# Kernel tuning notes

Hardware: AMD Instinct MI355X
Metric: run time of the kernel (lower is better)

Reference implementation:

```python
import jax, jax.numpy as jnp
import numpy as np

B, S, T = 32, 512, 32
EMB, HID = 256, 512
VOCAB, OOV = 50000, 100


def setup_inputs() -> dict:
    key = jax.random.key(0)
    ks = jax.random.split(key, 20)
    g = lambda k, shape: (0.02 * jax.random.normal(k, shape)).astype(jnp.float32)
    return {
        "dec_input_ids": jax.random.randint(ks[0], (B, T), 0, VOCAB),
        "enc_ids_ext": jax.random.randint(ks[1], (B, S), 0, VOCAB + OOV),
        "encoder_states": jax.random.normal(ks[2], (B, S, HID), jnp.float32),
        "enc_padding_mask": jnp.ones((B, S), jnp.float32),
        "init_h": jax.random.normal(ks[3], (B, HID), jnp.float32),
        "init_c": jax.random.normal(ks[4], (B, HID), jnp.float32),
        "embeddings": g(ks[5], (VOCAB, EMB)),
        "W_enc": g(ks[6], (HID, HID)),
        "b_enc": jnp.zeros((HID,), jnp.float32),
        "W_attn": g(ks[7], (2 * HID, HID)),
        "v": g(ks[8], (HID,)),
        "w_cov": g(ks[9], (HID,)),
        "b_cov": jnp.zeros((HID,), jnp.float32),
        "W_x": g(ks[10], (EMB + HID, HID)),
        "W_out": g(ks[11], (2 * HID, HID)),
        "Wk": g(ks[12], (HID, 4 * HID)),
        "Wr": g(ks[13], (HID, 4 * HID)),
        "b_lstm": jnp.zeros((4 * HID,), jnp.float32),
        "W_pgen": g(ks[14], (4 * HID, 1)),
        "W_proj": g(ks[15], (HID, VOCAB)),
        "b_proj": jnp.zeros((VOCAB,), jnp.float32),
    }


def reference(dec_input_ids, enc_ids_ext, encoder_states, enc_padding_mask,
              init_h, init_c, embeddings, W_enc, b_enc, W_attn, v, w_cov,
              b_cov, W_x, W_out, Wk, Wr, b_lstm, W_pgen, W_proj, b_proj):
    Bq = encoder_states.shape[0]
    # 1x1 conv over [B,S,1,H] == pointwise linear
    enc_feat = jnp.einsum('bsh,hv->bsv', encoder_states, W_enc) + b_enc  # [B,S,V]
    emb = jnp.swapaxes(embeddings[dec_input_ids], 0, 1)  # [T,B,E]
    rows = jnp.arange(Bq)[:, None]

    def lstm(x, h, c):
        z = x @ Wk + h @ Wr + b_lstm
        i, f, g_, o = jnp.split(z, 4, axis=-1)
        c2 = jax.nn.sigmoid(f) * c + jax.nn.sigmoid(i) * jnp.tanh(g_)
        h2 = jax.nn.sigmoid(o) * jnp.tanh(c2)
        return h2, c2

    def attend(h, c, cov):
        dec_feat = jnp.concatenate([h, c], -1) @ W_attn  # [B,V]
        feats = enc_feat + dec_feat[:, None, :]
        if cov is not None:  # 1x1 conv on coverage [B,S,1,1] -> [B,S,V]
            feats = feats + cov[..., None] * w_cov + b_cov
        e = jnp.sum(v * jnp.tanh(feats), -1)  # [B,S]
        attn = jax.nn.softmax(e, axis=-1) * enc_padding_mask
        attn = attn / jnp.sum(attn, -1, keepdims=True)
        ctx = jnp.einsum('bs,bsv->bv', attn, enc_feat)
        return ctx, attn

    def decode(inp, h, c, ctx, cov):
        x = jnp.concatenate([inp, ctx], -1) @ W_x
        h, c = lstm(x, h, c)
        ctx, attn = attend(h, c, cov)
        p_gen = jax.nn.sigmoid(jnp.concatenate([ctx, h, c, x], -1) @ W_pgen)  # [B,1]
        out = jnp.concatenate([h, ctx], -1) @ W_out
        vocab_dist = jax.nn.softmax(out @ W_proj + b_proj, axis=-1)
        ext = jnp.concatenate([p_gen * vocab_dist,
                               jnp.zeros((Bq, OOV), vocab_dist.dtype)], -1)
        final = ext.at[rows, enc_ids_ext].add((1.0 - p_gen) * attn)
        return h, c, ctx, attn, p_gen, final

    # step 0: coverage starts as None, initialized from first attn dist
    ctx0 = jnp.zeros((Bq, HID), encoder_states.dtype)
    h, c, ctx, attn0, pg0, final0 = decode(emb[0], init_h, init_c, ctx0, None)
    cov = attn0

    def scan_step(carry, inp):
        h, c, ctx, cov = carry
        h, c, ctx, attn, pg, final = decode(inp, h, c, ctx, cov)
        return (h, c, ctx, cov + attn), final

    (_, _, _, cov), finals = jax.lax.scan(scan_step, (h, c, ctx, cov), emb[1:])
    final_dists = jnp.concatenate([final0[None], finals], axis=0)  # [T,B,VOCAB+OOV]
    return final_dists
```

## Files before the change

kernel.cpp:

```cpp
#include <hip/hip_runtime.h>
#include <math.h>

#define Bq 32
#define Sq 512
#define Tq 32
#define EMBq 256
#define HIDq 512
#define VOCABq 50000
#define OOVq 100
#define VEXTq (VOCABq + OOVq)
#define HALF_N 25088

typedef unsigned short u16;
typedef unsigned long long u64;
typedef __attribute__((ext_vector_type(8))) short bf16x8;
typedef __attribute__((ext_vector_type(4))) float f32x4;

__device__ __forceinline__ float sigmoidf_(float x){ return 1.0f/(1.0f+__expf(-x)); }
__device__ __forceinline__ float tanhf_(float x){ return 1.0f - 2.0f/(__expf(2.0f*x)+1.0f); }

__device__ __forceinline__ u16 f2bf(float x){
  union{float f; unsigned u;} v; v.f=x;
  unsigned r = v.u + 0x7FFFu + ((v.u>>16)&1u);
  return (u16)(r>>16);
}
__device__ __forceinline__ float bf2f(u16 h){
  union{unsigned u; float f;} v; v.u = ((unsigned)h)<<16; return v.f;
}

__device__ __forceinline__ float ld1(const float* p){
  return __hip_atomic_load((float*)p, __ATOMIC_RELAXED, __HIP_MEMORY_SCOPE_AGENT);
}
__device__ __forceinline__ void st1(float* p, float v){
  __hip_atomic_store(p, v, __ATOMIC_RELAXED, __HIP_MEMORY_SCOPE_AGENT);
}
__device__ __forceinline__ float2 ld2(const float* p){
  u64 v = __hip_atomic_load((u64*)p, __ATOMIC_RELAXED, __HIP_MEMORY_SCOPE_AGENT);
  union{u64 u; float2 f;} c; c.u=v; return c.f;
}
__device__ __forceinline__ void atadd(float* p, float v){
  __hip_atomic_fetch_add(p, v, __ATOMIC_RELAXED, __HIP_MEMORY_SCOPE_AGENT);
}

__device__ __forceinline__ void mbar(unsigned* gs, int sc, unsigned tag){
  asm volatile("s_waitcnt vmcnt(0)" ::: "memory");
  __syncthreads();
  if (threadIdx.x==0)
    __hip_atomic_store(gs+sc, tag, __ATOMIC_RELAXED, __HIP_MEMORY_SCOPE_AGENT);
  if (threadIdx.x<64){
    for(;;){
      unsigned v = (threadIdx.x<8)
        ? __hip_atomic_load(gs+threadIdx.x, __ATOMIC_RELAXED, __HIP_MEMORY_SCOPE_AGENT)
        : tag;
      if (__all(v>=tag)) break;
      __builtin_amdgcn_s_sleep(1);
    }
  }
  __syncthreads();
}

__device__ __forceinline__ float blockSum512(float v, float* red){
  #pragma unroll
  for (int off=32; off>0; off>>=1) v += __shfl_down(v, off);
  int lane = threadIdx.x & 63, wid = threadIdx.x >> 6;
  __syncthreads();
  if (lane==0) red[wid]=v;
  __syncthreads();
  float t=0.f;
  #pragma unroll
  for (int w=0;w<8;++w) t+=red[w];
  return t;
}

__global__ __launch_bounds__(256) void k_wet(const float* __restrict__ W, u16* __restrict__ WT){
  __shared__ float T[32][33];
  const int n0 = blockIdx.x*32, k0 = blockIdx.y*32;
  const int tid=threadIdx.x;
  #pragma unroll
  for (int it=0; it<4; ++it){
    int id = tid+it*256; int kk=id>>5, nn=id&31;
    T[kk][nn] = W[(size_t)(k0+kk)*512 + n0+nn];
  }
  __syncthreads();
  #pragma unroll
  for (int it=0; it<4; ++it){
    int id=tid+it*256; int nn=id>>5, kk=id&31;
    WT[(size_t)(n0+nn)*512 + k0+kk] = f2bf(T[kk][nn]);
  }
}

__global__ __launch_bounds__(256) void k_wkt(const float* __restrict__ Wk, u16* __restrict__ WkT){
  __shared__ float T[32][33];
  const int n0 = blockIdx.x*32, k0 = blockIdx.y*32;
  const int tid=threadIdx.x;
  #pragma unroll
  for (int it=0; it<4; ++it){
    int id=tid+it*256; int kk=id>>5, nn=id&31;
    T[kk][nn] = Wk[(size_t)(k0+kk)*2048 + n0+nn];
  }
  __syncthreads();
  #pragma unroll
  for (int it=0; it<4; ++it){
    int id=tid+it*256; int nn=id>>5, kk=id&31;
    WkT[(size_t)(n0+nn)*512 + k0+kk] = f2bf(T[kk][nn]);
  }
}

__global__ __launch_bounds__(512) void k_wx2c(const float* __restrict__ W_x,
    const float* __restrict__ Wpgen, u16* __restrict__ Xb, float* __restrict__ Wxp){
  __shared__ float red[8];
  const int j = blockIdx.x, i = threadIdx.x;
  float v = W_x[(size_t)(256+j)*512 + i];
  Xb[(size_t)j*512 + i] = f2bf(v);
  float s = blockSum512(v*Wpgen[1536+i], red);
  if (i==0) Wxp[j] = s;
}

__global__ __launch_bounds__(256) void k_gemm512(const u16* __restrict__ A,
    const u16* __restrict__ B, const float* __restrict__ bias,
    float* __restrict__ out, int ncols, int use_bias){
  __shared__ u16 As[128*40];
  __shared__ u16 Bs[128*40];
  const int tid = threadIdx.x;
  const int m0 = blockIdx.x * 128;
  const int n0 = blockIdx.y * 128;
  const int wid = tid>>6, lane = tid&63;
  const int wm = (wid>>1)*64, wn = (wid&1)*64;
  const int l15 = lane&15, l4 = lane>>4;
  f32x4 acc[4][4];
  #pragma unroll
  for (int mi=0;mi<4;++mi)
    #pragma unroll
    for (int ni=0;ni<4;++ni) acc[mi][ni] = (f32x4){0.f,0.f,0.f,0.f};
  for (int kt=0; kt<16; ++kt){
    const int k0 = kt*32;
    __syncthreads();
    #pragma unroll
    for (int it=0; it<2; ++it){
      int id = tid + it*256;
      int row = id>>2, c4 = id&3;
      uint4 va = *(const uint4*)(A + (size_t)(m0+row)*512 + k0 + c4*8);
      *(uint4*)(&As[row*40 + c4*8]) = va;
      uint4 vb = *(const uint4*)(B + (size_t)(n0+row)*512 + k0 + c4*8);
      *(uint4*)(&Bs[row*40 + c4*8]) = vb;
    }
    __syncthreads();
    bf16x8 a[4], b[4];
    #pragma unroll
    for (int mi=0;mi<4;++mi) a[mi] = *(const bf16x8*)(&As[(wm+mi*16+l15)*40 + l4*8]);
    #pragma unroll
    for (int ni=0;ni<4;++ni) b[ni] = *(const bf16x8*)(&Bs[(wn+ni*16+l15)*40 + l4*8]);
    #pragma unroll
    for (int mi=0;mi<4;++mi)
      #pragma unroll
      for (int ni=0;ni<4;++ni)
        acc[mi][ni] = __builtin_amdgcn_mfma_f32_16x16x32_bf16(a[mi], b[ni], acc[mi][ni], 0,0,0);
  }
  #pragma unroll
  for (int ni=0;ni<4;++ni){
    const int col = n0 + wn + ni*16 + l15;
    const float bp = use_bias ? bias[col] : 0.f;
    #pragma unroll
    for (int mi=0;mi<4;++mi){
      const int rbase = m0 + wm + mi*16 + l4*4;
      #pragma unroll
      for (int r=0;r<4;++r)
        out[(size_t)(rbase+r)*ncols + col] = acc[mi][ni][r] + bp;
    }
  }
}

__global__ __launch_bounds__(256) void k_encm(const float* __restrict__ es,
    const u16* __restrict__ WET, const float* __restrict__ b_enc,
    u16* __restrict__ EFbf){
  __shared__ u16 As[128*40];
  __shared__ u16 Bs[128*40];
  const int tid=threadIdx.x;
  const int m0 = blockIdx.x*128, n0 = blockIdx.y*128;
  const int wid=tid>>6, lane=tid&63;
  const int wm=(wid>>1)*64, wn=(wid&1)*64;
  const int l15=lane&15, l4=lane>>4;
  f32x4 acc[4][4];
  #pragma unroll
  for (int mi=0;mi<4;++mi)
    #pragma unroll
    for (int ni=0;ni<4;++ni) acc[mi][ni] = (f32x4){0.f,0.f,0.f,0.f};
  for (int kt=0; kt<16; ++kt){
    const int k0=kt*32;
    __syncthreads();
    #pragma unroll
    for (int it=0; it<4; ++it){
      int id=tid+it*256; int row=id>>3, q=id&7;
      float4 v = *(const float4*)(es + (size_t)(m0+row)*512 + k0 + q*4);
      u64 pk = (u64)f2bf(v.x) | ((u64)f2bf(v.y)<<16) | ((u64)f2bf(v.z)<<32) | ((u64)f2bf(v.w)<<48);
      *(u64*)&As[row*40 + q*4] = pk;
    }
    #pragma unroll
    for (int it=0; it<2; ++it){
      int id=tid+it*256; int row=id>>2, c4=id&3;
      uint4 v = *(const uint4*)(WET + (size_t)(n0+row)*512 + k0 + c4*8);
      *(uint4*)&Bs[row*40 + c4*8] = v;
    }
    __syncthreads();
    bf16x8 a[4], b[4];
    #pragma unroll
    for (int mi=0;mi<4;++mi) a[mi] = *(const bf16x8*)(&As[(wm+mi*16+l15)*40 + l4*8]);
    #pragma unroll
    for (int ni=0;ni<4;++ni) b[ni] = *(const bf16x8*)(&Bs[(wn+ni*16+l15)*40 + l4*8]);
    #pragma unroll
    for (int mi=0;mi<4;++mi)
      #pragma unroll
      for (int ni=0;ni<4;++ni)
        acc[mi][ni] = __builtin_amdgcn_mfma_f32_16x16x32_bf16(a[mi], b[ni], acc[mi][ni], 0,0,0);
  }
  #pragma unroll
  for (int ni=0;ni<4;++ni){
    const int col = n0+wn+ni*16+l15;
    const float bp = b_enc[col];
    #pragma unroll
    for (int mi=0;mi<4;++mi){
      const int rb = m0+wm+mi*16+l4*4;
      #pragma unroll
      for (int r=0;r<4;++r)
        EFbf[(size_t)(rb+r)*512 + col] = f2bf(acc[mi][ni][r]+bp);
    }
  }
}

__global__ __launch_bounds__(512) void k_embx(const int* __restrict__ dec_ids,
  const float* __restrict__ emb, const float* __restrict__ W_x,
  const float* __restrict__ Wpgen, u16* __restrict__ embx_bf, float* __restrict__ embxp){
  __shared__ float A[16][257];
  __shared__ int ids[16];
  __shared__ float red[8];
  const int tid = threadIdx.x, r0 = blockIdx.x*16;
  if (tid<16){
    int row = r0+tid, tt = row>>5, bb = row&31;
    ids[tid] = dec_ids[bb*Tq + tt];
  }
  __syncthreads();
  for (int idx=tid; idx<16*256; idx+=512){
    int rr = idx>>8, kk = idx&255;
    A[rr][kk] = emb[(size_t)ids[rr]*EMBq + kk];
  }
  __syncthreads();
  float acc[16];
  #pragma unroll
  for (int r=0;r<16;++r) acc[r]=0.f;
  for (int k=0;k<256;++k){
    float w = W_x[(size_t)k*HIDq + tid];
    #pragma unroll
    for (int r=0;r<16;++r) acc[r] += A[r][k]*w;
  }
  float wp4 = Wpgen[1536+tid];
  for (int r=0;r<16;++r){
    embx_bf[(size_t)(r0+r)*HIDq + tid] = f2bf(acc[r]);
    float s = blockSum512(acc[r]*wp4, red);
    if (tid==0) embxp[r0+r] = s;
  }
}

__global__ __launch_bounds__(512) void k_trans(const float* __restrict__ in,
    float* __restrict__ out, int K, int N){
  __shared__ float T[32][33];
  const int n0 = blockIdx.x*32, k0 = blockIdx.y*32;
  const int tid = threadIdx.x;
  for (int idx=tid; idx<1024; idx+=512){
    int kk = idx>>5, nn = idx&31;
    T[kk][nn] = in[(size_t)(k0+kk)*N + n0+nn];
  }
  __syncthreads();
  for (int idx=tid; idx<1024; idx+=512){
    int nn = idx>>5, kk = idx&31;
    out[(size_t)(n0+nn)*K + k0+kk] = T[kk][nn];
  }
}

__global__ __launch_bounds__(512) void k_wgc(const float* __restrict__ WXKT_,
    const float* __restrict__ WrT_, u16* __restrict__ WGC){
  const int np = blockIdx.x;
  const int colg = np>>2, g = np&3;
  const int n = g*512 + colg;
  const int sc = np>>8, npl = np&255;
  u16* o = WGC + (size_t)sc*262144 + (size_t)npl*8;
  const int k = threadIdx.x;
  float v0 = WXKT_[(size_t)n*512 + k];
  float v1 = WrT_[(size_t)n*512 + k];
  o[(size_t)(k>>3)*2048 + (k&7)] = f2bf(v0);
  const int k2 = k + 512;
  o[(size_t)(k2>>3)*2048 + (k2&7)] = f2bf(v1);
}

__global__ void k_cvt(const float* __restrict__ in, u16* __restrict__ out, int n){
  int i = blockIdx.x*256 + threadIdx.x;
  if (i<n) out[i] = f2bf(in[i]);
}

__global__ __launch_bounds__(1024,1) void k_rec8(
  const u16* __restrict__ EFbf, const float* __restrict__ mask,
  const float* __restrict__ init_h, const float* __restrict__ init_c,
  const u16* __restrict__ WGC, const float* __restrict__ embz,
  const u16* __restrict__ WAbf, const float* __restrict__ vvec,
  const float* __restrict__ wcov, const float* __restrict__ bcov,
  const float* __restrict__ Wpgen, const float* __restrict__ Wxp,
  float* __restrict__ Hg, float* __restrict__ ctx_acc,
  float* __restrict__ df_acc, float* __restrict__ Z_acc,
  float* __restrict__ hc_ws, float* __restrict__ attn_ws,
  float* __restrict__ pgen_raw, unsigned* __restrict__ msl)
{
  __shared__ float xA[1024];
  __shared__ float zl4[4][256];
  __shared__ float zfin[256];
  __shared__ float hsl[64], csl[64];
  __shared__ float covb[64], wsv[64], coldv[64];
  __shared__ float dfp[1024];
  __shared__ float dfl[512];
  __shared__ float ctp[1024];
  __shared__ float el[64];
  __shared__ float Zsh;

  const int tid = threadIdx.x, bid = blockIdx.x;
  const int lane = tid&63, wv = tid>>6;
  const int sc = bid & 7, bB = bid >> 3, s0 = sc*64;
  const int j0l = lane*8;
  unsigned* gs = msl + bB*16;

  float vvr[8], wcr[8], bcr[8];
  *(float4*)&vvr[0] = *(const float4*)&vvec[j0l]; *(float4*)&vvr[4] = *(const float4*)&vvec[j0l+4];
  *(float4*)&wcr[0] = *(const float4*)&wcov[j0l]; *(float4*)&wcr[4] = *(const float4*)&wcov[j0l+4];
  *(float4*)&bcr[0] = *(const float4*)&bcov[j0l]; *(float4*)&bcr[4] = *(const float4*)&bcov[j0l+4];

  if (tid<64) csl[tid] = init_c[bB*512 + s0 + tid];

  const int colL = tid & 255;
  const int kq = tid >> 8;
  const u16* wbase = WGC + (size_t)sc*262144 + (size_t)(kq*32)*2048 + (size_t)colL*8;
  const float* xs = &xA[kq*256];

  unsigned mt = 0;

  for (int t=0; t<Tq; ++t){
    if (t==0){
      if (tid<512) xA[tid] = 0.f;
      else xA[tid] = init_h[bB*512 + (tid-512)];
      if (tid<64) st1(ctx_acc + bB*512 + s0+tid, 0.f);
      if (tid==0 && sc==0) st1(Z_acc + bB, 0.f);
      __syncthreads();
    } else {
      const int pr = (t-1)&1;
      float2 cf, hf; float Zl = 0.f;
      if (tid<256) cf = ld2(ctx_acc + (size_t)pr*16384 + bB*512 + tid*2);
      else if (tid<512) hf = ld2(Hg + (size_t)pr*16384 + bB*512 + (tid-256)*2);
      if (tid==0)  Zl = ld1(Z_acc + pr*32 + bB);
      if (tid<64)  coldv[tid] = xA[s0+tid];
      if (tid==0)  Zsh = Zl;
      __syncthreads();
      const float Z = Zsh;
      if (tid<256){ xA[tid*2] = cf.x/Z; xA[tid*2+1] = cf.y/Z; }
      else if (tid<512){ xA[512+(tid-256)*2] = hf.x; xA[512+(tid-256)*2+1] = hf.y; }
      __syncthreads();
      if (tid<64){
        const int j = s0+tid;
        float cxj = xA[j];
        __builtin_nontemporal_store(cxj, hc_ws + ((size_t)(t-1)*Bq+bB)*1024 + 512 + j);
        float a = wsv[tid]/Z;
        __builtin_nontemporal_store(a, attn_ws + ((size_t)(t-1)*Bq+bB)*Sq + j);
        covb[tid] = (t==1) ? a : covb[tid]+a;
        float part = cxj*Wpgen[j] + hsl[tid]*Wpgen[512+j]
                   + csl[tid]*Wpgen[1024+j] + coldv[tid]*Wxp[j];
        #pragma unroll
        for (int off=32; off>0; off>>=1) part += __shfl_down(part, off);
        if (tid==0) atadd(pgen_raw + (t-1)*Bq + bB, part);
      }
      if (tid<64) st1(ctx_acc + (size_t)(t&1)*16384 + bB*512 + s0+tid, 0.f);
      if (tid==0 && sc==0) st1(Z_acc + (t&1)*32 + bB, 0.f);
      __syncthreads();
    }
    {
      float acc = 0.f;
      #pragma unroll 8
      for (int kb=0; kb<32; ++kb){
        bf16x8 w8 = *(const bf16x8*)(wbase + (size_t)kb*2048);
        const u16* ph = (const u16*)&w8;
        float4 x0 = *(const float4*)(xs + kb*8);
        float4 x1 = *(const float4*)(xs + kb*8 + 4);
        acc += x0.x*bf2f(ph[0]) + x0.y*bf2f(ph[1]) + x0.z*bf2f(ph[2]) + x0.w*bf2f(ph[3])
             + x1.x*bf2f(ph[4]) + x1.y*bf2f(ph[5]) + x1.z*bf2f(ph[6]) + x1.w*bf2f(ph[7]);
      }
      zl4[kq][colL] = acc;
    }
    __syncthreads();
    if (tid<256) zfin[tid] = (zl4[0][tid]+zl4[1][tid]) + (zl4[2][tid]+zl4[3][tid]);
    __syncthreads();
    if (tid<64){
      const int colg = s0 + tid;
      const float* ez = embz + ((size_t)t*Bq + bB)*2048 + colg;
      float zi = zfin[tid*4+0] + __builtin_nontemporal_load(ez);
      float zf = zfin[tid*4+1] + __builtin_nontemporal_load(ez+512);
      float zg = zfin[tid*4+2] + __builtin_nontemporal_load(ez+1024);
      float zo = zfin[tid*4+3] + __builtin_nontemporal_load(ez+1536);
      float co = csl[tid];
      float cn = sigmoidf_(zf)*co + sigmoidf_(zi)*tanhf_(zg);
      float hn = sigmoidf_(zo)*tanhf_(cn);
      csl[tid] = cn;
      hsl[tid] = hn;
      st1(Hg + (size_t)(t&1)*16384 + bB*512 + colg, hn);
      __builtin_nontemporal_store(hn, hc_ws + ((size_t)t*Bq+bB)*1024 + colg);
    }
    __syncthreads();
    {
      const int j = tid & 511, half = tid >> 9;
      const float* st = half ? csl : hsl;
      const u16* wa = WAbf + (size_t)(half*512 + s0)*512 + j;
      float acc = 0.f;
      #pragma unroll 8
      for (int k=0;k<64;++k) acc += st[k]*bf2f(wa[(size_t)k*512]);
      dfp[tid] = acc;
    }
    __syncthreads();
    if (tid<512) atadd(df_acc + (size_t)(t&1)*16384 + bB*512 + tid, dfp[tid]+dfp[512+tid]);
    ++mt; mbar(gs, sc, mt);
    if (tid<256){
      float2 f = ld2(df_acc + (size_t)(t&1)*16384 + bB*512 + tid*2);
      dfl[tid*2]=f.x; dfl[tid*2+1]=f.y;
    } else if (tid>=960){
      st1(df_acc + (size_t)((t+1)&1)*16384 + bB*512 + s0 + (tid-960), 0.f);
    }
    __syncthreads();
    {
      float dd[8];
      *(float4*)&dd[0] = *(const float4*)&dfl[j0l];
      *(float4*)&dd[4] = *(const float4*)&dfl[j0l+4];
      const u16* efb = EFbf + ((size_t)(bB*512 + s0))*512;
      #pragma unroll
      for (int r=0;r<4;++r){
        int sl = wv*4 + r;
        uint4 pack = *(const uint4*)(efb + (size_t)sl*512 + j0l);
        const u16* ph = (const u16*)&pack;
        float a8 = 0.f;
        if (t>0){
          float cvs = covb[sl];
          #pragma unroll
          for (int q=0;q<8;++q) a8 += vvr[q]*tanhf_(bf2f(ph[q])+dd[q]+cvs*wcr[q]+bcr[q]);
        } else {
          #pragma unroll
          for (int q=0;q<8;++q) a8 += vvr[q]*tanhf_(bf2f(ph[q])+dd[q]);
        }
        #pragma unroll
        for (int off=32; off>0; off>>=1) a8 += __shfl_down(a8, off);
        if (lane==0) el[sl] = a8;
      }
    }
    __syncthreads();
    if (tid<64){
      float w_ = mask[bB*512+s0+tid]*__expf(el[tid]);
      wsv[tid] = w_;
      float Zc = w_;
      #pragma unroll
      for (int off=32; off>0; off>>=1) Zc += __shfl_xor(Zc, off);
      if (tid==0) atadd(Z_acc + (t&1)*32 + bB, Zc);
    }
    __syncthreads();
    {
      const int j = tid & 511, sh = tid >> 9;
      const u16* efc = EFbf + ((size_t)(bB*512 + s0 + sh*32))*512 + j;
      float acc = 0.f;
      #pragma unroll 4
      for (int s=0;s<32;++s) acc += wsv[sh*32+s]*bf2f(efc[(size_t)s*512]);
      ctp[tid] = acc;
    }
    __syncthreads();
    if (tid<512) atadd(ctx_acc + (size_t)(t&1)*16384 + bB*512 + tid, ctp[tid]+ctp[512+tid]);
    ++mt; mbar(gs, sc, mt);
  }
  {
    const int pr = (Tq-1)&1;
    float2 cf; float Zl = 0.f;
    if (tid<256) cf = ld2(ctx_acc + (size_t)pr*16384 + bB*512 + tid*2);
    if (tid==0)  Zl = ld1(Z_acc + pr*32 + bB);
    if (tid<64)  coldv[tid] = xA[s0+tid];
    if (tid==0)  Zsh = Zl;
    __syncthreads();
    const float Z = Zsh;
    if (tid<256){ xA[tid*2] = cf.x/Z; xA[tid*2+1] = cf.y/Z; }
    __syncthreads();
    if (tid<64){
      const int j = s0+tid;
      float cxj = xA[j];
      __builtin_nontemporal_store(cxj, hc_ws + ((size_t)(Tq-1)*Bq+bB)*1024 + 512 + j);
      float a = wsv[tid]/Z;
      __builtin_nontemporal_store(a, attn_ws + ((size_t)(Tq-1)*Bq+bB)*Sq + j);
      float part = cxj*Wpgen[j] + hsl[tid]*Wpgen[512+j]
                 + csl[tid]*Wpgen[1024+j] + coldv[tid]*Wxp[j];
      #pragma unroll
      for (int off=32; off>0; off>>=1) part += __shfl_down(part, off);
      if (tid==0) atadd(pgen_raw + (Tq-1)*Bq + bB, part);
    }
  }
}

__global__ __launch_bounds__(512) void k_mid(const float* __restrict__ hc,
    const float* __restrict__ W_out, u16* __restrict__ outm_bf){
  __shared__ float A[16][256];
  const int tid=threadIdx.x;
  const int r0=blockIdx.x*16;
  float acc[16];
  #pragma unroll
  for (int r=0;r<16;++r) acc[r]=0.f;
  for (int kc=0;kc<4;++kc){
    __syncthreads();
    for (int i=tid;i<16*256;i+=512){
      int rr=i>>8, kk=i&255;
      A[rr][kk]=hc[(size_t)(r0+rr)*1024 + kc*256+kk];
    }
    __syncthreads();
    for (int k=0;k<256;++k){
      float w=W_out[(size_t)(kc*256+k)*HIDq + tid];
      #pragma unroll
      for (int r=0;r<16;++r) acc[r]+=A[r][k]*w;
    }
  }
  #pragma unroll
  for (int r=0;r<16;++r) outm_bf[(size_t)(r0+r)*HIDq+tid]=f2bf(acc[r]);
}

__global__ __launch_bounds__(256) void k_wcvt(const float* __restrict__ Wp,
    u16* __restrict__ WT, int n_base){
  __shared__ float T[32][33];
  const int n0 = blockIdx.x*32, k0 = blockIdx.y*32;
  const int tid = threadIdx.x;
  #pragma unroll
  for (int it=0; it<4; ++it){
    int id = tid + it*256;
    int kk = id>>5, nn = id&31;
    int gn = n_base + n0 + nn;
    T[kk][nn] = (gn < VOCABq) ? Wp[(size_t)(k0+kk)*VOCABq + gn] : 0.f;
  }
  __syncthreads();
  #pragma unroll
  for (int it=0; it<4; ++it){
    int id = tid + it*256;
    int nn = id>>5, kk = id&31;
    WT[(size_t)(n0+nn)*512 + k0+kk] = f2bf(T[kk][nn]);
  }
}

__global__ __launch_bounds__(256) void k_projs(const u16* __restrict__ Abf,
    const u16* __restrict__ WT, const float* __restrict__ b_proj,
    float* __restrict__ out, float* __restrict__ rowsum, int n_base){
  __shared__ u16 As[128*40];
  __shared__ u16 Bs[128*40];
  const int tid = threadIdx.x;
  const int m0 = blockIdx.x * 128;
  const int n0 = blockIdx.y * 128;
  const int wid = tid>>6, lane = tid&63;
  const int wm = (wid>>1)*64, wn = (wid&1)*64;
  const int l15 = lane&15, l4 = lane>>4;
  f32x4 acc[4][4];
  #pragma unroll
  for (int mi=0;mi<4;++mi)
    #pragma unroll
    for (int ni=0;ni<4;++ni) acc[mi][ni] = (f32x4){0.f,0.f,0.f,0.f};

  for (int kt=0; kt<16; ++kt){
    const int k0 = kt*32;
    __syncthreads();
    #pragma unroll
    for (int it=0; it<2; ++it){
      int id = tid + it*256;
      int row = id>>2, c4 = id&3;
      uint4 va = *(const uint4*)(Abf + (size_t)(m0+row)*512 + k0 + c4*8);
      *(uint4*)(&As[row*40 + c4*8]) = va;
      uint4 vb = *(const uint4*)(WT + (size_t)(n0+row)*512 + k0 + c4*8);
      *(uint4*)(&Bs[row*40 + c4*8]) = vb;
    }
    __syncthreads();
    bf16x8 a[4], b[4];
    #pragma unroll
    for (int mi=0;mi<4;++mi)
      a[mi] = *(const bf16x8*)(&As[(wm + mi*16 + l15)*40 + l4*8]);
    #pragma unroll
    for (int ni=0;ni<4;++ni)
      b[ni] = *(const bf16x8*)(&Bs[(wn + ni*16 + l15)*40 + l4*8]);
    #pragma unroll
    for (int mi=0;mi<4;++mi)
      #pragma unroll
      for (int ni=0;ni<4;++ni)
        acc[mi][ni] = __builtin_amdgcn_mfma_f32_16x16x32_bf16(a[mi], b[ni], acc[mi][ni], 0,0,0);
  }

  float prow[4][4];
  #pragma unroll
  for (int mi=0;mi<4;++mi)
    #pragma unroll
    for (int r=0;r<4;++r) prow[mi][r]=0.f;

  #pragma unroll
  for (int ni=0;ni<4;++ni){
    const int col = n_base + n0 + wn + ni*16 + l15;
    const bool ok = (col < VOCABq);
    const float bp = ok ? b_proj[col] : 0.f;
    #pragma unroll
    for (int mi=0;mi<4;++mi){
      const int rbase = m0 + wm + mi*16 + l4*4;
      #pragma unroll
      for (int r=0;r<4;++r){
        float p = ok ? __expf(acc[mi][ni][r] + bp) : 0.f;
        if (ok) out[(size_t)(rbase+r)*VEXTq + col] = p;
        prow[mi][r] += p;
      }
    }
  }
  #pragma unroll
  for (int mi=0;mi<4;++mi)
    #pragma unroll
    for (int r=0;r<4;++r){
      float v = prow[mi][r];
      v += __shfl_xor(v,1); v += __shfl_xor(v,2);
      v += __shfl_xor(v,4); v += __shfl_xor(v,8);
      if (l15==0) atadd(rowsum + m0 + wm + mi*16 + l4*4 + r, v);
    }
}

__global__ __launch_bounds__(256) void k_sm2(float* __restrict__ out,
    const float* __restrict__ rowsum, const float* __restrict__ pgen_raw,
    const float* __restrict__ embxp, const float* __restrict__ attn_ws,
    const int* __restrict__ enc_ids){
  const int row=blockIdx.x, tid=threadIdx.x;
  const int b = row & (Bq-1);
  float* orow = out + (size_t)row*VEXTq;
  const float pg = sigmoidf_(pgen_raw[row] + embxp[row]);
  const float scale = pg / rowsum[row];
  float4* o4 = (float4*)orow;
  for (int i=tid;i<VOCABq/4;i+=256){
    float4 v = o4[i];
    v.x*=scale; v.y*=scale; v.z*=scale; v.w*=scale;
    o4[i] = v;
  }
  for (int i=VOCABq+tid;i<VEXTq;i+=256) orow[i] = 0.f;
  __syncthreads();
  const float w1 = 1.f-pg;
  const float* arow = attn_ws + (size_t)row*Sq;
  const int* ids = enc_ids + b*Sq;
  for (int si=tid; si<Sq; si+=256)
    atomicAdd(&orow[ids[si]], w1*arow[si]);
}

extern "C" void kernel_launch(void* const* d_in, const int* in_sizes, int n_in,
                              void* d_out, int out_size, void* d_ws, size_t ws_size,
                              hipStream_t stream) {
  (void)in_sizes; (void)n_in; (void)out_size; (void)ws_size;
  const int*   dec_ids    = (const int*)  d_in[0];
  const int*   enc_ids    = (const int*)  d_in[1];
  const float* enc_states = (const float*)d_in[2];
  const float* mask       = (const float*)d_in[3];
  const float* init_h     = (const float*)d_in[4];
  const float* init_c     = (const float*)d_in[5];
  const float* embeddings = (const float*)d_in[6];
  const float* W_enc      = (const float*)d_in[7];
  const float* b_enc      = (const float*)d_in[8];
  const float* W_attn     = (const float*)d_in[9];
  const float* vvec       = (const float*)d_in[10];
  const float* w_cov      = (const float*)d_in[11];
  const float* b_cov      = (const float*)d_in[12];
  const float* W_x        = (const float*)d_in[13];
  const float* W_out      = (const float*)d_in[14];
  const float* Wk         = (const float*)d_in[15];
  const float* Wr         = (const float*)d_in[16];
  const float* b_lstm     = (const float*)d_in[17];
  const float* W_pgen     = (const float*)d_in[18];
  const float* W_proj     = (const float*)d_in[19];
  const float* b_proj     = (const float*)d_in[20];
  float* out = (float*)d_out;
  float* ws  = (float*)d_ws;

  u16*   EFbf    = (u16*)ws;
  float* attn_ws = ws + 4194304;
  float* hc_ws   = attn_ws + 524288;
  u16*   outm_bf = (u16*)(hc_ws + 1048576);
  u16*   embx_bf = (u16*)(hc_ws + 1048576 + 262144);
  float* embxp   = hc_ws + 1048576 + 262144 + 262144;
  float* embz    = embxp + 1024;
  float* WXKT_   = embz + 2097152;
  float* WrT_    = WXKT_ + 1048576;
  u16*   WkT     = (u16*)(WrT_ + 1048576);
  u16*   Xb      = (u16*)(((float*)WkT) + 524288);
  float* Wxp     = ((float*)Xb) + 131072;
  float* Hg      = Wxp + 512;
  unsigned* msl  = (unsigned*)(Hg + 32768);
  float* pgen_raw= (float*)(msl + 512);
  float* ctx_acc = pgen_raw + 1024;
  float* df_acc  = ctx_acc + 32768;
  float* Z_acc   = df_acc + 32768;
  float* rowsum  = Z_acc + 64;
  u16*   WGC     = (u16*)(rowsum + 1024);
  u16*   WAbf    = (u16*)(((float*)WGC) + 1048576);
  u16*   WET     = (u16*)(((float*)WAbf) + 262144);
  u16*   WT      = (u16*)(((float*)WET) + 131072);

  hipMemsetAsync(msl, 0, (512 + 1024 + 32768 + 32768 + 64 + 1024)*sizeof(unsigned), stream);

  {
    dim3 g(16,16);
    k_wet<<<g, 256, 0, stream>>>(W_enc, WET);
  }
  {
    dim3 g(128,4);
    k_encm<<<g, 256, 0, stream>>>(enc_states, WET, b_enc, EFbf);
  }
  k_embx<<<64, 512, 0, stream>>>(dec_ids, embeddings, W_x, W_pgen, embx_bf, embxp);
  {
    dim3 g(64,16);
    k_wkt<<<g, 256, 0, stream>>>(Wk, WkT);
  }
  k_wx2c<<<512, 512, 0, stream>>>(W_x, W_pgen, Xb, Wxp);
  {
    dim3 g(8,16);
    k_gemm512<<<g, 256, 0, stream>>>(embx_bf, WkT, b_lstm, embz, 2048, 1);
  }
  {
    dim3 g(16,4);
    k_gemm512<<<g, 256, 0, stream>>>(WkT, Xb, (const float*)0, WXKT_, 512, 0);
  }
  {
    dim3 g(64,16);
    k_trans<<<g, 512, 0, stream>>>(Wr, WrT_, 512, 2048);
  }
  k_wgc<<<2048, 512, 0, stream>>>(WXKT_, WrT_, WGC);
  k_cvt<<<(524288+255)/256, 256, 0, stream>>>(W_attn, WAbf, 524288);

  {
    void* args[] = { (void*)&EFbf, (void*)&mask, (void*)&init_h, (void*)&init_c,
                     (void*)&WGC, (void*)&embz, (void*)&WAbf, (void*)&vvec,
                     (void*)&w_cov, (void*)&b_cov, (void*)&W_pgen, (void*)&Wxp,
                     (void*)&Hg, (void*)&ctx_acc, (void*)&df_acc, (void*)&Z_acc,
                     (void*)&hc_ws, (void*)&attn_ws, (void*)&pgen_raw,
                     (void*)&msl };
    hipLaunchCooperativeKernel((void*)k_rec8, dim3(256), dim3(1024), args, 0, stream);
  }

  k_mid<<<(Tq*Bq)/16, 512, 0, stream>>>(hc_ws, W_out, outm_bf);
  for (int half=0; half<2; ++half){
    const int n_base = half*HALF_N;
    dim3 gc(HALF_N/32, 16);
    k_wcvt<<<gc, 256, 0, stream>>>(W_proj, WT, n_base);
    dim3 gp(8, HALF_N/128);
    k_projs<<<gp, 256, 0, stream>>>(outm_bf, WT, b_proj, out, rowsum, n_base);
  }
  k_sm2<<<Tq*Bq, 256, 0, stream>>>(out, rowsum, pgen_raw, embxp, attn_ws, enc_ids);
}
```

Baseline: 1.584 ms.

## Replace scalar W_out GEMM with bf16 MFMA and fuse weight-prep kernels

```diff
diff --git a/kernel.cpp b/kernel.cpp
--- a/kernel.cpp
+++ b/kernel.cpp
@@ -72,37 +72,35 @@
   return t;
 }
 
-__global__ __launch_bounds__(256) void k_wet(const float* __restrict__ W, u16* __restrict__ WT){
+__global__ __launch_bounds__(256) void k_prep(
+    const float* __restrict__ W_enc, u16* __restrict__ WET,
+    const float* __restrict__ Wk,    u16* __restrict__ WkT,
+    const float* __restrict__ W_out, u16* __restrict__ WoT,
+    const float* __restrict__ W_attn,u16* __restrict__ WAbf){
   __shared__ float T[32][33];
-  const int n0 = blockIdx.x*32, k0 = blockIdx.y*32;
-  const int tid=threadIdx.x;
-  #pragma unroll
-  for (int it=0; it<4; ++it){
-    int id = tid+it*256; int kk=id>>5, nn=id&31;
-    T[kk][nn] = W[(size_t)(k0+kk)*512 + n0+nn];
-  }
-  __syncthreads();
-  #pragma unroll
-  for (int it=0; it<4; ++it){
-    int id=tid+it*256; int nn=id>>5, kk=id&31;
-    WT[(size_t)(n0+nn)*512 + k0+kk] = f2bf(T[kk][nn]);
-  }
-}
-
-__global__ __launch_bounds__(256) void k_wkt(const float* __restrict__ Wk, u16* __restrict__ WkT){
-  __shared__ float T[32][33];
-  const int n0 = blockIdx.x*32, k0 = blockIdx.y*32;
-  const int tid=threadIdx.x;
-  #pragma unroll
-  for (int it=0; it<4; ++it){
-    int id=tid+it*256; int kk=id>>5, nn=id&31;
-    T[kk][nn] = Wk[(size_t)(k0+kk)*2048 + n0+nn];
-  }
-  __syncthreads();
-  #pragma unroll
-  for (int it=0; it<4; ++it){
-    int id=tid+it*256; int nn=id>>5, kk=id&31;
-    WkT[(size_t)(n0+nn)*512 + k0+kk] = f2bf(T[kk][nn]);
+  const int bid = blockIdx.x, tid = threadIdx.x;
+  if (bid < 1792){
+    const float* in; u16* out; int ldin, ldout, n0, k0;
+    if (bid < 256){ in=W_enc; out=WET; ldin=512; ldout=512;
+      n0=(bid&15)*32; k0=(bid>>4)*32; }
+    else if (bid < 1280){ int b=bid-256; in=Wk; out=WkT; ldin=2048; ldout=512;
+      n0=(b&63)*32; k0=(b>>6)*32; }
+    else { int b=bid-1280; in=W_out; out=WoT; ldin=512; ldout=1024;
+      n0=(b&15)*32; k0=(b>>4)*32; }
+    #pragma unroll
+    for (int it=0; it<4; ++it){
+      int id=tid+it*256; int kk=id>>5, nn=id&31;
+      T[kk][nn] = in[(size_t)(k0+kk)*ldin + n0+nn];
+    }
+    __syncthreads();
+    #pragma unroll
+    for (int it=0; it<4; ++it){
+      int id=tid+it*256; int nn=id>>5, kk=id&31;
+      out[(size_t)(n0+nn)*ldout + k0+kk] = f2bf(T[kk][nn]);
+    }
+  } else {
+    int i = (bid-1792)*256 + tid;
+    WAbf[i] = f2bf(W_attn[i]);
   }
 }
 
@@ -166,6 +164,59 @@
       #pragma unroll
       for (int r=0;r<4;++r)
         out[(size_t)(rbase+r)*ncols + col] = acc[mi][ni][r] + bp;
+    }
+  }
+}
+
+__global__ __launch_bounds__(256) void k_gemmb(const u16* __restrict__ A,
+    const u16* __restrict__ B, u16* __restrict__ out, int K, int N){
+  __shared__ u16 As[128*40];
+  __shared__ u16 Bs[128*40];
+  const int tid = threadIdx.x;
+  const int m0 = blockIdx.x * 128;
+  const int n0 = blockIdx.y * 128;
+  const int wid = tid>>6, lane = tid&63;
+  const int wm = (wid>>1)*64, wn = (wid&1)*64;
+  const int l15 = lane&15, l4 = lane>>4;
+  f32x4 acc[4][4];
+  #pragma unroll
+  for (int mi=0;mi<4;++mi)
+    #pragma unroll
+    for (int ni=0;ni<4;++ni) acc[mi][ni] = (f32x4){0.f,0.f,0.f,0.f};
+  const int kts = K>>5;
+  for (int kt=0; kt<kts; ++kt){
+    const int k0 = kt*32;
+    __syncthreads();
+    #pragma unroll
+    for (int it=0; it<2; ++it){
+      int id = tid + it*256;
+      int row = id>>2, c4 = id&3;
+      uint4 va = *(const uint4*)(A + (size_t)(m0+row)*K + k0 + c4*8);
+      *(uint4*)(&As[row*40 + c4*8]) = va;
+      uint4 vb = *(const uint4*)(B + (size_t)(n0+row)*K + k0 + c4*8);
+      *(uint4*)(&Bs[row*40 + c4*8]) = vb;
+    }
+    __syncthreads();
+    bf16x8 a[4], b[4];
+    #pragma unroll
+    for (int mi=0;mi<4;++mi) a[mi] = *(const bf16x8*)(&As[(wm+mi*16+l15)*40 + l4*8]);
+    #pragma unroll
+    for (int ni=0;ni<4;++ni) b[ni] = *(const bf16x8*)(&Bs[(wn+ni*16+l15)*40 + l4*8]);
+    #pragma unroll
+    for (int mi=0;mi<4;++mi)
+      #pragma unroll
+      for (int ni=0;ni<4;++ni)
+        acc[mi][ni] = __builtin_amdgcn_mfma_f32_16x16x32_bf16(a[mi], b[ni], acc[mi][ni], 0,0,0);
+  }
+  #pragma unroll
+  for (int ni=0;ni<4;++ni){
+    const int col = n0 + wn + ni*16 + l15;
+    #pragma unroll
+    for (int mi=0;mi<4;++mi){
+      const int rbase = m0 + wm + mi*16 + l4*4;
+      #pragma unroll
+      for (int r=0;r<4;++r)
+        out[(size_t)(rbase+r)*N + col] = f2bf(acc[mi][ni][r]);
     }
   }
 }
@@ -291,12 +342,7 @@
   o[(size_t)(k2>>3)*2048 + (k2&7)] = f2bf(v1);
 }
 
-__global__ void k_cvt(const float* __restrict__ in, u16* __restrict__ out, int n){
-  int i = blockIdx.x*256 + threadIdx.x;
-  if (i<n) out[i] = f2bf(in[i]);
-}
-
-__global__ __launch_bounds__(1024,1) void k_rec8(
+__global__ __launch_bounds__(1024,1) void k_rec9(
   const u16* __restrict__ EFbf, const float* __restrict__ mask,
   const float* __restrict__ init_h, const float* __restrict__ init_c,
   const u16* __restrict__ WGC, const float* __restrict__ embz,
@@ -305,12 +351,11 @@
   const float* __restrict__ Wpgen, const float* __restrict__ Wxp,
   float* __restrict__ Hg, float* __restrict__ ctx_acc,
   float* __restrict__ df_acc, float* __restrict__ Z_acc,
-  float* __restrict__ hc_ws, float* __restrict__ attn_ws,
+  u16* __restrict__ hc_bf, float* __restrict__ attn_ws,
   float* __restrict__ pgen_raw, unsigned* __restrict__ msl)
 {
   __shared__ float xA[1024];
   __shared__ float zl4[4][256];
-  __shared__ float zfin[256];
   __shared__ float hsl[64], csl[64];
   __shared__ float covb[64], wsv[64], coldv[64];
   __shared__ float dfp[1024];
@@ -362,7 +407,7 @@
       if (tid<64){
         const int j = s0+tid;
         float cxj = xA[j];
-        __builtin_nontemporal_store(cxj, hc_ws + ((size_t)(t-1)*Bq+bB)*1024 + 512 + j);
+        __builtin_nontemporal_store(f2bf(cxj), hc_bf + ((size_t)(t-1)*Bq+bB)*1024 + 512 + j);
         float a = wsv[tid]/Z;
         __builtin_nontemporal_store(a, attn_ws + ((size_t)(t-1)*Bq+bB)*Sq + j);
         covb[tid] = (t==1) ? a : covb[tid]+a;
@@ -390,22 +435,24 @@
       zl4[kq][colL] = acc;
     }
     __syncthreads();
-    if (tid<256) zfin[tid] = (zl4[0][tid]+zl4[1][tid]) + (zl4[2][tid]+zl4[3][tid]);
-    __syncthreads();
     if (tid<64){
       const int colg = s0 + tid;
       const float* ez = embz + ((size_t)t*Bq + bB)*2048 + colg;
-      float zi = zfin[tid*4+0] + __builtin_nontemporal_load(ez);
-      float zf = zfin[tid*4+1] + __builtin_nontemporal_load(ez+512);
-      float zg = zfin[tid*4+2] + __builtin_nontemporal_load(ez+1024);
-      float zo = zfin[tid*4+3] + __builtin_nontemporal_load(ez+1536);
+      float zi = (zl4[0][tid*4+0]+zl4[1][tid*4+0])+(zl4[2][tid*4+0]+zl4[3][tid*4+0])
+               + __builtin_nontemporal_load(ez);
+      float zf = (zl4[0][tid*4+1]+zl4[1][tid*4+1])+(zl4[2][tid*4+1]+zl4[3][tid*4+1])
+               + __builtin_nontemporal_load(ez+512);
+      float zg = (zl4[0][tid*4+2]+zl4[1][tid*4+2])+(zl4[2][tid*4+2]+zl4[3][tid*4+2])
+               + __builtin_nontemporal_load(ez+1024);
+      float zo = (zl4[0][tid*4+3]+zl4[1][tid*4+3])+(zl4[2][tid*4+3]+zl4[3][tid*4+3])
+               + __builtin_nontemporal_load(ez+1536);
       float co = csl[tid];
       float cn = sigmoidf_(zf)*co + sigmoidf_(zi)*tanhf_(zg);
       float hn = sigmoidf_(zo)*tanhf_(cn);
       csl[tid] = cn;
       hsl[tid] = hn;
       st1(Hg + (size_t)(t&1)*16384 + bB*512 + colg, hn);
-      __builtin_nontemporal_store(hn, hc_ws + ((size_t)t*Bq+bB)*1024 + colg);
+      __builtin_nontemporal_store(f2bf(hn), hc_bf + ((size_t)t*Bq+bB)*1024 + colg);
     }
     __syncthreads();
     {
@@ -487,7 +534,7 @@
     if (tid<64){
       const int j = s0+tid;
       float cxj = xA[j];
-      __builtin_nontemporal_store(cxj, hc_ws + ((size_t)(Tq-1)*Bq+bB)*1024 + 512 + j);
+      __builtin_nontemporal_store(f2bf(cxj), hc_bf + ((size_t)(Tq-1)*Bq+bB)*1024 + 512 + j);
       float a = wsv[tid]/Z;
       __builtin_nontemporal_store(a, attn_ws + ((size_t)(Tq-1)*Bq+bB)*Sq + j);
       float part = cxj*Wpgen[j] + hsl[tid]*Wpgen[512+j]
@@ -497,31 +544,6 @@
       if (tid==0) atadd(pgen_raw + (Tq-1)*Bq + bB, part);
     }
   }
-}
-
-__global__ __launch_bounds__(512) void k_mid(const float* __restrict__ hc,
-    const float* __restrict__ W_out, u16* __restrict__ outm_bf){
-  __shared__ float A[16][256];
-  const int tid=threadIdx.x;
-  const int r0=blockIdx.x*16;
-  float acc[16];
-  #pragma unroll
-  for (int r=0;r<16;++r) acc[r]=0.f;
-  for (int kc=0;kc<4;++kc){
-    __syncthreads();
-    for (int i=tid;i<16*256;i+=512){
-      int rr=i>>8, kk=i&255;
-      A[rr][kk]=hc[(size_t)(r0+rr)*1024 + kc*256+kk];
-    }
-    __syncthreads();
-    for (int k=0;k<256;++k){
-      float w=W_out[(size_t)(kc*256+k)*HIDq + tid];
-      #pragma unroll
-      for (int r=0;r<16;++r) acc[r]+=A[r][k]*w;
-    }
-  }
-  #pragma unroll
-  for (int r=0;r<16;++r) outm_bf[(size_t)(r0+r)*HIDq+tid]=f2bf(acc[r]);
 }
 
 __global__ __launch_bounds__(256) void k_wcvt(const float* __restrict__ Wp,
@@ -676,16 +698,17 @@
 
   u16*   EFbf    = (u16*)ws;
   float* attn_ws = ws + 4194304;
-  float* hc_ws   = attn_ws + 524288;
-  u16*   outm_bf = (u16*)(hc_ws + 1048576);
-  u16*   embx_bf = (u16*)(hc_ws + 1048576 + 262144);
-  float* embxp   = hc_ws + 1048576 + 262144 + 262144;
+  u16*   hc_bf   = (u16*)(attn_ws + 524288);
+  u16*   outm_bf = (u16*)(attn_ws + 524288 + 524288);
+  u16*   embx_bf = (u16*)(attn_ws + 524288 + 524288 + 262144);
+  float* embxp   = attn_ws + 524288 + 524288 + 262144 + 262144;
   float* embz    = embxp + 1024;
   float* WXKT_   = embz + 2097152;
   float* WrT_    = WXKT_ + 1048576;
   u16*   WkT     = (u16*)(WrT_ + 1048576);
   u16*   Xb      = (u16*)(((float*)WkT) + 524288);
-  float* Wxp     = ((float*)Xb) + 131072;
+  u16*   WoT     = (u16*)(((float*)Xb) + 131072);
+  float* Wxp     = ((float*)WoT) + 262144;
   float* Hg      = Wxp + 512;
   unsigned* msl  = (unsigned*)(Hg + 32768);
   float* pgen_raw= (float*)(msl + 512);
@@ -700,19 +723,12 @@
 
   hipMemsetAsync(msl, 0, (512 + 1024 + 32768 + 32768 + 64 + 1024)*sizeof(unsigned), stream);
 
-  {
-    dim3 g(16,16);
-    k_wet<<<g, 256, 0, stream>>>(W_enc, WET);
-  }
+  k_prep<<<3840, 256, 0, stream>>>(W_enc, WET, Wk, WkT, W_out, WoT, W_attn, WAbf);
   {
     dim3 g(128,4);
     k_encm<<<g, 256, 0, stream>>>(enc_states, WET, b_enc, EFbf);
   }
   k_embx<<<64, 512, 0, stream>>>(dec_ids, embeddings, W_x, W_pgen, embx_bf, embxp);
-  {
-    dim3 g(64,16);
-    k_wkt<<<g, 256, 0, stream>>>(Wk, WkT);
-  }
   k_wx2c<<<512, 512, 0, stream>>>(W_x, W_pgen, Xb, Wxp);
   {
     dim3 g(8,16);
@@ -727,19 +743,21 @@
     k_trans<<<g, 512, 0, stream>>>(Wr, WrT_, 512, 2048);
   }
   k_wgc<<<2048, 512, 0, stream>>>(WXKT_, WrT_, WGC);
-  k_cvt<<<(524288+255)/256, 256, 0, stream>>>(W_attn, WAbf, 524288);
 
   {
     void* args[] = { (void*)&EFbf, (void*)&mask, (void*)&init_h, (void*)&init_c,
                      (void*)&WGC, (void*)&embz, (void*)&WAbf, (void*)&vvec,
                      (void*)&w_cov, (void*)&b_cov, (void*)&W_pgen, (void*)&Wxp,
                      (void*)&Hg, (void*)&ctx_acc, (void*)&df_acc, (void*)&Z_acc,
-                     (void*)&hc_ws, (void*)&attn_ws, (void*)&pgen_raw,
+                     (void*)&hc_bf, (void*)&attn_ws, (void*)&pgen_raw,
                      (void*)&msl };
-    hipLaunchCooperativeKernel((void*)k_rec8, dim3(256), dim3(1024), args, 0, stream);
-  }
-
-  k_mid<<<(Tq*Bq)/16, 512, 0, stream>>>(hc_ws, W_out, outm_bf);
+    hipLaunchCooperativeKernel((void*)k_rec9, dim3(256), dim3(1024), args, 0, stream);
+  }
+
+  {
+    dim3 g(8,4);
+    k_gemmb<<<g, 256, 0, stream>>>(hc_bf, WoT, outm_bf, 1024, 512);
+  }
   for (int half=0; half<2; ++half){
     const int n_base = half*HALF_N;
     dim3 gc(HALF_N/32, 16);
```

Result: faster. 1.425 ms (-10.1%).
